# Kernel optimization log

Measured on AMD Instinct MI355X. Metric: run time of the kernel, lower is better.

Reference implementation:

```python
import jax, jax.numpy as jnp
import numpy as np

NBINS = 256
HMIN, HMAX = 0.0, 255.0

def _histc(x, nbins=NBINS, lo=HMIN, hi=HMAX):
    # Faithful torch.histc: bin width (hi-lo)/nbins; values outside [lo,hi] ignored;
    # values == hi fall into the last bin. Returns float counts.
    xf = x.reshape(-1)
    width = (hi - lo) / nbins
    idx = jnp.floor((xf - lo) / width).astype(jnp.int32)
    idx = jnp.minimum(idx, nbins - 1)            # x == hi -> last bin
    in_range = (xf >= lo) & (xf <= hi)
    idx = jnp.where(in_range, idx, nbins)        # out-of-range -> dropped bucket
    hist = jnp.zeros(nbins + 1, dtype=x.dtype).at[idx].add(1.0)
    return hist[:nbins]

def setup_inputs() -> dict:
    key = jax.random.key(0)
    # intensity image with values in [0, 255]
    x = jax.random.uniform(key, (8192, 4096), dtype=jnp.float32) * 255.0
    return {"batchsize": 16, "input": x}

def reference(batchsize, input):
    hist = _histc(input)                          # [256] float counts
    # Original loop recomputes the same histc each iter and does
    # count += hist[0] (scalar broadcast into all 256 slots).
    count = jnp.zeros(NBINS, dtype=hist.dtype) + jnp.asarray(batchsize, hist.dtype) * hist[0]
    return (hist, count)
```

## Files before the change

### kernel.cpp

```cpp
#include <hip/hip_runtime.h>

#define NBINS 256
#define BLOCK 64
#define CNT_DW (64 * 64)
#define BIN_SCALE (256.0f / 255.0f)
#define TARGET_G 2560
#define MAX_K 61

__global__ void zero_out(float* __restrict__ out) {
    const int i = blockIdx.x * blockDim.x + threadIdx.x;
    if (i < 2 * NBINS) out[i] = 0.0f;
}

__device__ __forceinline__ void classify(float v, int t, int& dw, unsigned& inc) {
    int idx = (int)(v * BIN_SCALE);
    idx = idx < 255 ? idx : 255;
    const bool ok = (v >= 0.0f) && (v <= 255.0f);
    dw = ok ? (((((unsigned)idx) >> 2) << 6) + t) : t;
    inc = ok ? (1u << ((idx & 3) << 3)) : 0u;
}

__global__ __launch_bounds__(BLOCK) void hist_kernel(const float* __restrict__ x,
                                                     unsigned int* __restrict__ partial,
                                                     float* __restrict__ out,
                                                     int n, int G, int use_ws) {
    __shared__ unsigned int cnt[CNT_DW];
    const int t = threadIdx.x;

    {
        uint4* z4 = (uint4*)cnt;
#pragma unroll
        for (int i = 0; i < CNT_DW / 4 / BLOCK; ++i)
            z4[t + i * BLOCK] = make_uint4(0u, 0u, 0u, 0u);
    }
    __syncthreads();

    const int n4 = n >> 2;
    const float4* __restrict__ x4 = (const float4*)x;
    const int S = G * BLOCK;
    const int i0 = blockIdx.x * BLOCK + t;
    const int K = n4 / S;

    if (K > 0) {
        float4 v = x4[i0];
        float4 nxt = (K > 1) ? x4[i0 + S] : v;

        int pd0, pd1, pd2, pd3; unsigned ps0, ps1, ps2, ps3;
        classify(v.x, t, pd0, ps0);
        classify(v.y, t, pd1, ps1);
        classify(v.z, t, pd2, ps2);
        classify(v.w, t, pd3, ps3);
        unsigned po0 = cnt[pd0], po1 = cnt[pd1], po2 = cnt[pd2], po3 = cnt[pd3];

        for (int k = 1; k < K; ++k) {
            v = nxt;
            const int pa = (k + 1 < K) ? (i0 + (k + 1) * S) : i0;
            nxt = x4[pa];

            int d0, d1, d2, d3; unsigned s0, s1, s2, s3;
            classify(v.x, t, d0, s0);
            classify(v.y, t, d1, s1);
            classify(v.z, t, d2, s2);
            classify(v.w, t, d3, s3);

            unsigned w0 = po0 + ps0;
            unsigned w1 = po1 + ps1 + (pd1 == pd0 ? ps0 : 0u);
            unsigned w2 = po2 + ps2 + (pd2 == pd0 ? ps0 : 0u) + (pd2 == pd1 ? ps1 : 0u);
            unsigned w3 = po3 + ps3 + (pd3 == pd0 ? ps0 : 0u) + (pd3 == pd1 ? ps1 : 0u)
                                    + (pd3 == pd2 ? ps2 : 0u);
            cnt[pd0] = w0; cnt[pd1] = w1; cnt[pd2] = w2; cnt[pd3] = w3;

            po0 = cnt[d0]; po1 = cnt[d1]; po2 = cnt[d2]; po3 = cnt[d3];
            pd0 = d0; pd1 = d1; pd2 = d2; pd3 = d3;
            ps0 = s0; ps1 = s1; ps2 = s2; ps3 = s3;
        }
        unsigned w0 = po0 + ps0;
        unsigned w1 = po1 + ps1 + (pd1 == pd0 ? ps0 : 0u);
        unsigned w2 = po2 + ps2 + (pd2 == pd0 ? ps0 : 0u) + (pd2 == pd1 ? ps1 : 0u);
        unsigned w3 = po3 + ps3 + (pd3 == pd0 ? ps0 : 0u) + (pd3 == pd1 ? ps1 : 0u)
                                + (pd3 == pd2 ? ps2 : 0u);
        cnt[pd0] = w0; cnt[pd1] = w1; cnt[pd2] = w2; cnt[pd3] = w3;
    }

    {
        const int it = i0 + K * S;
        if (it < n4) {
            float4 v = x4[it];
            int d; unsigned s;
            classify(v.x, t, d, s); cnt[d] += s;
            classify(v.y, t, d, s); cnt[d] += s;
            classify(v.z, t, d, s); cnt[d] += s;
            classify(v.w, t, d, s); cnt[d] += s;
        }
    }
    for (int j = (n4 << 2) + i0; j < n; j += S) {
        int d; unsigned s;
        classify(x[j], t, d, s);
        cnt[d] += s;
    }
    __syncthreads();

    unsigned accA = 0, accB = 0;
#pragma unroll 16
    for (int k = 0; k < 64; ++k) {
        unsigned u = cnt[(t << 6) + ((t + k) & 63)];
        accA += u & 0x00FF00FFu;
        accB += (u >> 8) & 0x00FF00FFu;
    }
    const unsigned b0 = accA & 0xFFFFu, b2 = accA >> 16;
    const unsigned b1 = accB & 0xFFFFu, b3 = accB >> 16;

    if (use_ws) {
        ((uint4*)(partial + (size_t)blockIdx.x * NBINS))[t] = make_uint4(b0, b1, b2, b3);
    } else {
        if (b0) atomicAdd(&out[4 * t + 0], (float)b0);
        if (b1) atomicAdd(&out[4 * t + 1], (float)b1);
        if (b2) atomicAdd(&out[4 * t + 2], (float)b2);
        if (b3) atomicAdd(&out[4 * t + 3], (float)b3);
    }
}

__global__ __launch_bounds__(NBINS) void reduce_kernel(const unsigned int* __restrict__ partial,
                                                       float* __restrict__ out,
                                                       int G, int slice) {
    const int bin = threadIdx.x;
    const int g0 = blockIdx.x * slice;
    const int g1 = (g0 + slice < G) ? (g0 + slice) : G;
    unsigned s = 0;
    for (int g = g0; g < g1; ++g)
        s += partial[(size_t)g * NBINS + bin];
    if (s) atomicAdd(&out[bin], (float)s);
}

__global__ void count_kernel(const void* __restrict__ bs_raw,
                             float* __restrict__ out) {
    const int as_int = *(const int*)bs_raw;
    float bs;
    if (as_int >= 1 && as_int < (1 << 20)) {
        bs = (float)as_int;
    } else {
        bs = *(const float*)bs_raw;
    }
    out[NBINS + threadIdx.x] = bs * out[0];
}

extern "C" void kernel_launch(void* const* d_in, const int* in_sizes, int n_in,
                              void* d_out, int out_size, void* d_ws, size_t ws_size,
                              hipStream_t stream) {
    const void* bs_ptr;
    const float* x;
    int n;
    if (n_in >= 2 && in_sizes[0] == 1) {
        bs_ptr = d_in[0];
        x = (const float*)d_in[1];
        n = in_sizes[1];
    } else {
        bs_ptr = d_in[1];
        x = (const float*)d_in[0];
        n = in_sizes[0];
    }

    float* out = (float*)d_out;
    unsigned int* partial = (unsigned int*)d_ws;

    const long n4 = (long)n >> 2;
    long Gmin = (n4 + (long)BLOCK * MAX_K - 1) / ((long)BLOCK * MAX_K);
    int G = (int)(Gmin > TARGET_G ? Gmin : TARGET_G);
    if (G < 1) G = 1;

    const size_t ws_need = (size_t)G * NBINS * sizeof(unsigned int);
    const int use_ws = (ws_size >= ws_need) ? 1 : 0;

    zero_out<<<2, 256, 0, stream>>>(out);
    hist_kernel<<<G, BLOCK, 0, stream>>>(x, partial, out, n, G, use_ws);
    if (use_ws) {
        const int slice = (G + NBINS - 1) / NBINS;
        reduce_kernel<<<NBINS, NBINS, 0, stream>>>(partial, out, G, slice);
    }
    count_kernel<<<1, NBINS, 0, stream>>>(bs_ptr, out);
}
```

Baseline: 223.6 us.

## Enlarge histogram blocks to 256 threads and prefetch two loads ahead

```diff
diff --git a/kernel.cpp b/kernel.cpp
--- a/kernel.cpp
+++ b/kernel.cpp
@@ -1,11 +1,11 @@
 #include <hip/hip_runtime.h>
 
 #define NBINS 256
-#define BLOCK 64
-#define CNT_DW (64 * 64)
+#define BLOCK 256
+#define CNT_DW (64 * BLOCK)
 #define BIN_SCALE (256.0f / 255.0f)
-#define TARGET_G 2560
-#define MAX_K 61
+#define TARGET_G 1024
+#define MAX_PER_THREAD 240
 
 __global__ void zero_out(float* __restrict__ out) {
     const int i = blockIdx.x * blockDim.x + threadIdx.x;
@@ -16,7 +16,7 @@
     int idx = (int)(v * BIN_SCALE);
     idx = idx < 255 ? idx : 255;
     const bool ok = (v >= 0.0f) && (v <= 255.0f);
-    dw = ok ? (((((unsigned)idx) >> 2) << 6) + t) : t;
+    dw = ok ? ((((unsigned)idx >> 2) << 8) + t) : t;
     inc = ok ? (1u << ((idx & 3) << 3)) : 0u;
 }
 
@@ -39,41 +39,55 @@
     const float4* __restrict__ x4 = (const float4*)x;
     const int S = G * BLOCK;
     const int i0 = blockIdx.x * BLOCK + t;
-    const int K = n4 / S;
+    const int K = (i0 < n4) ? ((n4 - i0 + S - 1) / S) : 0;
+
+    int pd0 = t, pd1 = t, pd2 = t, pd3 = t;
+    unsigned ps0 = 0, ps1 = 0, ps2 = 0, ps3 = 0;
+    unsigned po0 = 0, po1 = 0, po2 = 0, po3 = 0;
+    bool have_p = false;
+
+    auto process = [&](const float4& v) {
+        int d0, d1, d2, d3; unsigned s0, s1, s2, s3;
+        classify(v.x, t, d0, s0);
+        classify(v.y, t, d1, s1);
+        classify(v.z, t, d2, s2);
+        classify(v.w, t, d3, s3);
+        unsigned w0 = po0 + ps0;
+        unsigned w1 = po1 + ps1 + (pd1 == pd0 ? ps0 : 0u);
+        unsigned w2 = po2 + ps2 + (pd2 == pd0 ? ps0 : 0u) + (pd2 == pd1 ? ps1 : 0u);
+        unsigned w3 = po3 + ps3 + (pd3 == pd0 ? ps0 : 0u) + (pd3 == pd1 ? ps1 : 0u)
+                                + (pd3 == pd2 ? ps2 : 0u);
+        cnt[pd0] = w0; cnt[pd1] = w1; cnt[pd2] = w2; cnt[pd3] = w3;
+        po0 = cnt[d0]; po1 = cnt[d1]; po2 = cnt[d2]; po3 = cnt[d3];
+        pd0 = d0; pd1 = d1; pd2 = d2; pd3 = d3;
+        ps0 = s0; ps1 = s1; ps2 = s2; ps3 = s3;
+    };
 
     if (K > 0) {
-        float4 v = x4[i0];
-        float4 nxt = (K > 1) ? x4[i0 + S] : v;
+        have_p = true;
+        float4 A = x4[i0];
+        process(A);
 
-        int pd0, pd1, pd2, pd3; unsigned ps0, ps1, ps2, ps3;
-        classify(v.x, t, pd0, ps0);
-        classify(v.y, t, pd1, ps1);
-        classify(v.z, t, pd2, ps2);
-        classify(v.w, t, pd3, ps3);
-        unsigned po0 = cnt[pd0], po1 = cnt[pd1], po2 = cnt[pd2], po3 = cnt[pd3];
-
-        for (int k = 1; k < K; ++k) {
-            v = nxt;
-            const int pa = (k + 1 < K) ? (i0 + (k + 1) * S) : i0;
-            nxt = x4[pa];
-
-            int d0, d1, d2, d3; unsigned s0, s1, s2, s3;
-            classify(v.x, t, d0, s0);
-            classify(v.y, t, d1, s1);
-            classify(v.z, t, d2, s2);
-            classify(v.w, t, d3, s3);
-
-            unsigned w0 = po0 + ps0;
-            unsigned w1 = po1 + ps1 + (pd1 == pd0 ? ps0 : 0u);
-            unsigned w2 = po2 + ps2 + (pd2 == pd0 ? ps0 : 0u) + (pd2 == pd1 ? ps1 : 0u);
-            unsigned w3 = po3 + ps3 + (pd3 == pd0 ? ps0 : 0u) + (pd3 == pd1 ? ps1 : 0u)
-                                    + (pd3 == pd2 ? ps2 : 0u);
-            cnt[pd0] = w0; cnt[pd1] = w1; cnt[pd2] = w2; cnt[pd3] = w3;
-
-            po0 = cnt[d0]; po1 = cnt[d1]; po2 = cnt[d2]; po3 = cnt[d3];
-            pd0 = d0; pd1 = d1; pd2 = d2; pd3 = d3;
-            ps0 = s0; ps1 = s1; ps2 = s2; ps3 = s3;
+        if (K >= 3) {
+            float4 B = x4[i0 + S];
+            float4 C = x4[i0 + 2 * S];
+            int k = 1;
+            for (; k + 1 < K; k += 2) {
+                float4 nb = x4[i0 + (k + 2 < K ? (k + 2) : 0) * S];
+                process(B);
+                float4 nc = x4[i0 + (k + 3 < K ? (k + 3) : 0) * S];
+                process(C);
+                B = nb; C = nc;
+            }
+            if (k < K) process(B);
+        } else {
+            for (int k = 1; k < K; ++k) {
+                float4 B = x4[i0 + k * S];
+                process(B);
+            }
         }
+    }
+    if (have_p) {
         unsigned w0 = po0 + ps0;
         unsigned w1 = po1 + ps1 + (pd1 == pd0 ? ps0 : 0u);
         unsigned w2 = po2 + ps2 + (pd2 == pd0 ? ps0 : 0u) + (pd2 == pd1 ? ps1 : 0u);
@@ -82,17 +96,6 @@
         cnt[pd0] = w0; cnt[pd1] = w1; cnt[pd2] = w2; cnt[pd3] = w3;
     }
 
-    {
-        const int it = i0 + K * S;
-        if (it < n4) {
-            float4 v = x4[it];
-            int d; unsigned s;
-            classify(v.x, t, d, s); cnt[d] += s;
-            classify(v.y, t, d, s); cnt[d] += s;
-            classify(v.z, t, d, s); cnt[d] += s;
-            classify(v.w, t, d, s); cnt[d] += s;
-        }
-    }
     for (int j = (n4 << 2) + i0; j < n; j += S) {
         int d; unsigned s;
         classify(x[j], t, d, s);
@@ -100,23 +103,31 @@
     }
     __syncthreads();
 
+    const int q = t >> 2;
+    const int p = t & 3;
     unsigned accA = 0, accB = 0;
 #pragma unroll 16
-    for (int k = 0; k < 64; ++k) {
-        unsigned u = cnt[(t << 6) + ((t + k) & 63)];
+    for (int j = 0; j < 64; ++j) {
+        unsigned u = cnt[(q << 8) + (p << 6) + ((j + t) & 63)];
         accA += u & 0x00FF00FFu;
         accB += (u >> 8) & 0x00FF00FFu;
     }
-    const unsigned b0 = accA & 0xFFFFu, b2 = accA >> 16;
-    const unsigned b1 = accB & 0xFFFFu, b3 = accB >> 16;
+    accA += __shfl_xor(accA, 1, 64);
+    accA += __shfl_xor(accA, 2, 64);
+    accB += __shfl_xor(accB, 1, 64);
+    accB += __shfl_xor(accB, 2, 64);
 
-    if (use_ws) {
-        ((uint4*)(partial + (size_t)blockIdx.x * NBINS))[t] = make_uint4(b0, b1, b2, b3);
-    } else {
-        if (b0) atomicAdd(&out[4 * t + 0], (float)b0);
-        if (b1) atomicAdd(&out[4 * t + 1], (float)b1);
-        if (b2) atomicAdd(&out[4 * t + 2], (float)b2);
-        if (b3) atomicAdd(&out[4 * t + 3], (float)b3);
+    if (p == 0) {
+        const unsigned b0 = accA & 0xFFFFu, b2 = accA >> 16;
+        const unsigned b1 = accB & 0xFFFFu, b3 = accB >> 16;
+        if (use_ws) {
+            ((uint4*)(partial + (size_t)blockIdx.x * NBINS))[q] = make_uint4(b0, b1, b2, b3);
+        } else {
+            if (b0) atomicAdd(&out[4 * q + 0], (float)b0);
+            if (b1) atomicAdd(&out[4 * q + 1], (float)b1);
+            if (b2) atomicAdd(&out[4 * q + 2], (float)b2);
+            if (b3) atomicAdd(&out[4 * q + 3], (float)b3);
+        }
     }
 }
 
@@ -163,8 +174,7 @@
     float* out = (float*)d_out;
     unsigned int* partial = (unsigned int*)d_ws;
 
-    const long n4 = (long)n >> 2;
-    long Gmin = (n4 + (long)BLOCK * MAX_K - 1) / ((long)BLOCK * MAX_K);
+    long Gmin = ((long)n + (long)BLOCK * MAX_PER_THREAD - 1) / ((long)BLOCK * MAX_PER_THREAD);
     int G = (int)(Gmin > TARGET_G ? Gmin : TARGET_G);
     if (G < 1) G = 1;
 
```

Result: faster. 204.6 us (-8.5%).
